# Performance work log

Hardware: AMD Instinct MI355X
Metric: run time of the kernel (lower is better)

The kernel has to match this reference:

```python
import jax, jax.numpy as jnp
import numpy as np

N_NODES = 50000
N_EDGES = 800000
DIM = 128
BN_EPS = 1e-5  # torch.nn.BatchNorm1d default


def _lin_init(k, fan_in, fan_out):
    kw, kb = jax.random.split(k)
    s = 1.0 / np.sqrt(fan_in)
    W = jax.random.uniform(kw, (fan_in, fan_out), jnp.float32, -s, s)
    b = jax.random.uniform(kb, (fan_out,), jnp.float32, -s, s)
    return W, b


def setup_inputs() -> dict:
    key = jax.random.key(0)
    ks = jax.random.split(key, 8)
    d = {}
    d['h'] = jax.random.normal(ks[0], (N_NODES, DIM), jnp.float32)
    d['e'] = jax.random.normal(ks[1], (N_EDGES, DIM), jnp.float32)
    d['src'] = jax.random.randint(ks[2], (N_EDGES,), 0, N_NODES)
    d['dst'] = jax.random.randint(ks[3], (N_EDGES,), 0, N_NODES)
    # mlp_atom: Linear(128,128) -> ReLU -> Linear(128,128)
    d['Wa1'], d['ba1'] = _lin_init(ks[4], DIM, DIM)
    d['Wa2'], d['ba2'] = _lin_init(ks[5], DIM, DIM)
    # mlp_bond
    d['Wb1'], d['bb1'] = _lin_init(ks[6], DIM, DIM)
    d['Wb2'], d['bb2'] = _lin_init(ks[7], DIM, DIM)
    # BatchNorm1d affine params
    d['gamma_a'] = jnp.ones((DIM,), jnp.float32)
    d['beta_a'] = jnp.zeros((DIM,), jnp.float32)
    d['gamma_b'] = jnp.ones((DIM,), jnp.float32)
    d['beta_b'] = jnp.zeros((DIM,), jnp.float32)
    return d


def _mlp(x, W1, b1, W2, b2):
    return jax.nn.relu(x @ W1 + b1) @ W2 + b2


def _bn(x, gamma, beta):
    # training-mode batch norm over the node/edge axis
    mu = jnp.mean(x, axis=0)
    var = jnp.var(x, axis=0)
    return (x - mu) * jax.lax.rsqrt(var + BN_EPS) * gamma + beta


def reference(h, e, src, dst, Wa1, ba1, Wa2, ba2, Wb1, bb1, Wb2, bb2,
              gamma_a, beta_a, gamma_b, beta_b):
    # --- bond (edge) update: GIN-style sum of endpoint atom feats + bond feat
    me = h[src] + h[dst] + e                      # [E, D] irregular gather
    e_new = _bn(_mlp(me, Wb1, bb1, Wb2, bb2), gamma_b, beta_b)
    e_new = e_new + e                             # residual (dropout=Identity)
    # --- atom (node) update: sum-aggregate incident bond feats
    agg = jax.ops.segment_sum(e_new, dst, num_segments=N_NODES)  # [N, D] scatter
    h_new = _bn(_mlp(h + agg, Wa1, ba1, Wa2, ba2), gamma_a, beta_a)
    h_new = h_new + h                             # residual
    return h_new, e_new
```

## Files before the change

kernel.cpp:

```cpp
#include <hip/hip_runtime.h>
#include <cstddef>

#define NN 50000
#define NE 800000
#define D 128
#define BN_EPS 1e-5f

typedef __attribute__((ext_vector_type(8))) short bf16x8;
typedef __attribute__((ext_vector_type(4))) float f32x4;
typedef __attribute__((ext_vector_type(4))) unsigned short us4;

__device__ __forceinline__ unsigned short f2bf(float x) {
    unsigned u = __float_as_uint(x);
    return (unsigned short)((u + 0x7fffu + ((u >> 16) & 1u)) >> 16);
}
__device__ __forceinline__ float bf2f(unsigned short b) {
    return __uint_as_float(((unsigned)b) << 16);
}

__global__ __launch_bounds__(256) void wprep_kernel(
    const float* __restrict__ W, unsigned short* __restrict__ Wt)
{
    const int idx = blockIdx.x * 256 + threadIdx.x;
    const int j  = idx & 7;
    const int l  = (idx >> 3) & 63;
    const int ks = (idx >> 9) & 3;
    const int ct = (idx >> 11) & 7;
    const int n  = 16 * ct + (l & 15);
    const int k  = 32 * ks + ((l >> 4) << 3) + j;
    Wt[idx] = f2bf(W[k * 128 + n]);
}

template<int MODE>
__global__ __launch_bounds__(256, 2) void mlp_mfma_kernel(
    const float* __restrict__ h, const float* __restrict__ e_or_agg,
    const int* __restrict__ src, const int* __restrict__ dst,
    const unsigned short* __restrict__ Wt1, const float* __restrict__ b1,
    const unsigned short* __restrict__ Wt2, const float* __restrict__ b2,
    float* __restrict__ x2out, float* __restrict__ stats)
{
    __shared__ __align__(16) unsigned short Xh[8192];
    __shared__ __align__(16) unsigned short Xl[8192];
    __shared__ __align__(16) float OUTB[64 * 132];

    const int tid  = threadIdx.x;
    const int lane = tid & 63;
    const int w    = tid >> 6;
    const int cg   = tid & 31;
    const int rg   = tid >> 5;
    const int c0   = cg * 4;
    const long r0  = (long)blockIdx.x * 64;

    const bf16x8* Wg1 = (const bf16x8*)Wt1;
    bf16x8 wf[8][4];
#pragma unroll
    for (int ct = 0; ct < 8; ++ct)
#pragma unroll
        for (int ks = 0; ks < 4; ++ks)
            wf[ct][ks] = Wg1[(ct * 4 + ks) * 64 + lane];

#pragma unroll
    for (int p = 0; p < 8; ++p) {
        const int  row  = p * 8 + rg;
        const long grow = r0 + row;
        float4 v = make_float4(0.f, 0.f, 0.f, 0.f);
        if (MODE == 0) {
            const int sN = src[grow];
            const int dN = dst[grow];
            const float4 ev = *(const float4*)(e_or_agg + (size_t)grow * D + c0);
            const float4 hs = *(const float4*)(h + (size_t)sN * D + c0);
            const float4 hd = *(const float4*)(h + (size_t)dN * D + c0);
            v.x = ev.x + hs.x + hd.x; v.y = ev.y + hs.y + hd.y;
            v.z = ev.z + hs.z + hd.z; v.w = ev.w + hs.w + hd.w;
        } else {
            if (grow < NN) {
                const float4 hv = *(const float4*)(h + (size_t)grow * D + c0);
                const float4 av = *(const float4*)(e_or_agg + (size_t)grow * D + c0);
                v.x = hv.x + av.x; v.y = hv.y + av.y;
                v.z = hv.z + av.z; v.w = hv.w + av.w;
            }
        }
        us4 hi, lo;
        hi.x = f2bf(v.x); lo.x = f2bf(v.x - bf2f(hi.x));
        hi.y = f2bf(v.y); lo.y = f2bf(v.y - bf2f(hi.y));
        hi.z = f2bf(v.z); lo.z = f2bf(v.z - bf2f(hi.z));
        hi.w = f2bf(v.w); lo.w = f2bf(v.w - bf2f(hi.w));
        const int addr = row * 128 + (((c0 >> 3) ^ (row & 7)) << 3) + (c0 & 7);
        *(us4*)&Xh[addr] = hi;
        *(us4*)&Xl[addr] = lo;
    }
    __syncthreads();

    const int arow = 16 * w + (lane & 15);
    bf16x8 ah[4], al[4];
#pragma unroll
    for (int ks = 0; ks < 4; ++ks) {
        const int col0  = 32 * ks + ((lane >> 4) << 3);
        const int aaddr = arow * 128 + (((col0 >> 3) ^ (arow & 7)) << 3);
        ah[ks] = *(const bf16x8*)&Xh[aaddr];
        al[ks] = *(const bf16x8*)&Xl[aaddr];
    }
    f32x4 acc[8];
#pragma unroll
    for (int ct = 0; ct < 8; ++ct) acc[ct] = (f32x4){0.f, 0.f, 0.f, 0.f};
#pragma unroll
    for (int ct = 0; ct < 8; ++ct)
#pragma unroll
        for (int ks = 0; ks < 4; ++ks) {
            acc[ct] = __builtin_amdgcn_mfma_f32_16x16x32_bf16(ah[ks], wf[ct][ks], acc[ct], 0, 0, 0);
            acc[ct] = __builtin_amdgcn_mfma_f32_16x16x32_bf16(al[ks], wf[ct][ks], acc[ct], 0, 0, 0);
        }

    const bf16x8* Wg2 = (const bf16x8*)Wt2;
#pragma unroll
    for (int ct = 0; ct < 8; ++ct)
#pragma unroll
        for (int ks = 0; ks < 4; ++ks)
            wf[ct][ks] = Wg2[(ct * 4 + ks) * 64 + lane];

#pragma unroll
    for (int ct = 0; ct < 8; ++ct) {
        const float b1c = b1[16 * ct + (lane & 15)];
#pragma unroll
        for (int r = 0; r < 4; ++r) {
            const int row = 16 * w + ((lane >> 4) << 2) + r;
            OUTB[row * 132 + 16 * ct + (lane & 15)] = fmaxf(acc[ct][r] + b1c, 0.f);
        }
    }
    __syncthreads();

#pragma unroll
    for (int p = 0; p < 8; ++p) {
        const int row = p * 8 + rg;
        const float4 v = *(const float4*)&OUTB[row * 132 + c0];
        us4 hi, lo;
        hi.x = f2bf(v.x); lo.x = f2bf(v.x - bf2f(hi.x));
        hi.y = f2bf(v.y); lo.y = f2bf(v.y - bf2f(hi.y));
        hi.z = f2bf(v.z); lo.z = f2bf(v.z - bf2f(hi.z));
        hi.w = f2bf(v.w); lo.w = f2bf(v.w - bf2f(hi.w));
        const int addr = row * 128 + (((c0 >> 3) ^ (row & 7)) << 3) + (c0 & 7);
        *(us4*)&Xh[addr] = hi;
        *(us4*)&Xl[addr] = lo;
    }
    __syncthreads();

#pragma unroll
    for (int ks = 0; ks < 4; ++ks) {
        const int col0  = 32 * ks + ((lane >> 4) << 3);
        const int aaddr = arow * 128 + (((col0 >> 3) ^ (arow & 7)) << 3);
        ah[ks] = *(const bf16x8*)&Xh[aaddr];
        al[ks] = *(const bf16x8*)&Xl[aaddr];
    }
    f32x4 a2[8];
#pragma unroll
    for (int ct = 0; ct < 8; ++ct) a2[ct] = (f32x4){0.f, 0.f, 0.f, 0.f};
#pragma unroll
    for (int ct = 0; ct < 8; ++ct)
#pragma unroll
        for (int ks = 0; ks < 4; ++ks) {
            a2[ct] = __builtin_amdgcn_mfma_f32_16x16x32_bf16(ah[ks], wf[ct][ks], a2[ct], 0, 0, 0);
            a2[ct] = __builtin_amdgcn_mfma_f32_16x16x32_bf16(al[ks], wf[ct][ks], a2[ct], 0, 0, 0);
        }

#pragma unroll
    for (int ct = 0; ct < 8; ++ct) {
        const float b2c = b2[16 * ct + (lane & 15)];
#pragma unroll
        for (int r = 0; r < 4; ++r) {
            const int row = 16 * w + ((lane >> 4) << 2) + r;
            OUTB[row * 132 + 16 * ct + (lane & 15)] = a2[ct][r] + b2c;
        }
    }
    __syncthreads();

    float ts[4] = {0.f, 0.f, 0.f, 0.f};
    float tq[4] = {0.f, 0.f, 0.f, 0.f};
#pragma unroll
    for (int p = 0; p < 8; ++p) {
        const int  row  = p * 8 + rg;
        const long grow = r0 + row;
        if (MODE == 1 && grow >= NN) continue;
        const float4 v = *(const float4*)&OUTB[row * 132 + c0];
        *(float4*)(x2out + (size_t)grow * D + c0) = v;
        ts[0] += v.x; ts[1] += v.y; ts[2] += v.z; ts[3] += v.w;
        tq[0] += v.x * v.x; tq[1] += v.y * v.y;
        tq[2] += v.z * v.z; tq[3] += v.w * v.w;
    }

    float* red = (float*)Xh;
    *(float4*)&red[rg * 128 + c0]        = make_float4(ts[0], ts[1], ts[2], ts[3]);
    *(float4*)&red[2048 + rg * 128 + c0] = make_float4(tq[0], tq[1], tq[2], tq[3]);
    __syncthreads();
    if (tid < 128) {
        float s = 0.f, q = 0.f;
#pragma unroll
        for (int g = 0; g < 8; ++g) {
            s += red[g * 128 + tid];
            q += red[2048 + g * 128 + tid];
        }
        unsafeAtomicAdd(&stats[tid], s);
        unsafeAtomicAdd(&stats[128 + tid], q);
    }
}

__global__ void bn_finalize_kernel(float* __restrict__ stats,
                                   const float* __restrict__ gamma,
                                   const float* __restrict__ beta,
                                   float inv_count)
{
    const int c = threadIdx.x;
    if (c < D) {
        const float mu  = stats[c] * inv_count;
        const float var = stats[128 + c] * inv_count - mu * mu;
        const float sc  = rsqrtf(var + BN_EPS) * gamma[c];
        stats[256 + c] = sc;
        stats[384 + c] = beta[c] - mu * sc;
    }
}

__global__ __launch_bounds__(256) void hist_kernel(
    const int* __restrict__ dst, int* __restrict__ cnt)
{
    const int i = blockIdx.x * 256 + threadIdx.x;
    if (i < NE) atomicAdd(&cnt[dst[i]], 1);
}

__global__ __launch_bounds__(1024) void scan_kernel(
    const int* __restrict__ cnt, int* __restrict__ off)
{
    __shared__ int part[1024];
    const int t = threadIdx.x;
    const int SEG = (NN + 1023) / 1024;
    const int base = t * SEG;

    int s = 0;
    for (int i = 0; i < SEG; ++i) {
        const int idx = base + i;
        if (idx < NN) s += cnt[idx];
    }
    part[t] = s;
    __syncthreads();
    for (int d = 1; d < 1024; d <<= 1) {
        int v = (t >= d) ? part[t - d] : 0;
        __syncthreads();
        part[t] += v;
        __syncthreads();
    }
    int run = (t > 0) ? part[t - 1] : 0;
    for (int i = 0; i < SEG; ++i) {
        const int idx = base + i;
        if (idx < NN) { off[idx] = run; run += cnt[idx]; }
    }
    if (t == 1023) off[NN] = part[1023];
}

__global__ __launch_bounds__(256) void csr_scatter_kernel(
    const int* __restrict__ dst, const int* __restrict__ off,
    int* __restrict__ cnt, int* __restrict__ csr)
{
    const int i = blockIdx.x * 256 + threadIdx.x;
    if (i < NE) {
        const int d = dst[i];
        const int p = atomicSub(&cnt[d], 1) - 1;
        csr[off[d] + p] = i;
    }
}

__global__ __launch_bounds__(256) void apply_gather_kernel(
    const float* __restrict__ e, const float* __restrict__ stats,
    const int* __restrict__ off, const int* __restrict__ csr,
    float* __restrict__ eout, float* __restrict__ agg)
{
    const int node = blockIdx.x * 4 + (threadIdx.x >> 6);
    const int lane = threadIdx.x & 63;
    const int c0   = lane * 2;
    if (node >= NN) return;

    const float2 sc = *(const float2*)(stats + 256 + c0);
    const float2 sh = *(const float2*)(stats + 384 + c0);
    float2 acc = make_float2(0.f, 0.f);
    const int jb = off[node], je = off[node + 1];
    for (int j = jb; j < je; ++j) {
        const int eidx = csr[j];
        const size_t base = (size_t)eidx * D + c0;
        const float2 x  = *(const float2*)(eout + base);
        const float2 ev = *(const float2*)(e + base);
        float2 v;
        v.x = fmaf(x.x, sc.x, sh.x) + ev.x;
        v.y = fmaf(x.y, sc.y, sh.y) + ev.y;
        *(float2*)(eout + base) = v;
        acc.x += v.x;
        acc.y += v.y;
    }
    *(float2*)(agg + (size_t)node * D + c0) = acc;
}

__global__ __launch_bounds__(256) void node_apply_kernel(
    const float* __restrict__ h, const float* __restrict__ stats,
    float* __restrict__ hout)
{
    const int gid = blockIdx.x * 256 + threadIdx.x;
    const int c0  = (gid & 31) * 4;
    const size_t base = (size_t)(gid >> 5) * D + c0;

    const float4 sc = *(const float4*)(stats + 256 + c0);
    const float4 sh = *(const float4*)(stats + 384 + c0);
    const float4 x  = *(const float4*)(hout + base);
    const float4 hv = *(const float4*)(h + base);
    float4 v;
    v.x = fmaf(x.x, sc.x, sh.x) + hv.x;
    v.y = fmaf(x.y, sc.y, sh.y) + hv.y;
    v.z = fmaf(x.z, sc.z, sh.z) + hv.z;
    v.w = fmaf(x.w, sc.w, sh.w) + hv.w;
    *(float4*)(hout + base) = v;
}

extern "C" void kernel_launch(void* const* d_in, const int* in_sizes, int n_in,
                              void* d_out, int out_size, void* d_ws, size_t ws_size,
                              hipStream_t stream)
{
    const float* h   = (const float*)d_in[0];
    const float* e   = (const float*)d_in[1];
    const int*   src = (const int*)d_in[2];
    const int*   dst = (const int*)d_in[3];
    const float* Wa1 = (const float*)d_in[4];
    const float* ba1 = (const float*)d_in[5];
    const float* Wa2 = (const float*)d_in[6];
    const float* ba2 = (const float*)d_in[7];
    const float* Wb1 = (const float*)d_in[8];
    const float* bb1 = (const float*)d_in[9];
    const float* Wb2 = (const float*)d_in[10];
    const float* bb2 = (const float*)d_in[11];
    const float* ga  = (const float*)d_in[12];
    const float* bea = (const float*)d_in[13];
    const float* gb  = (const float*)d_in[14];
    const float* beb = (const float*)d_in[15];

    float* out  = (float*)d_out;
    float* hnew = out;
    float* enew = out + (size_t)NN * D;

    float* ws     = (float*)d_ws;
    float* estats = ws;
    float* nstats = ws + 512;
    int*   icnt   = (int*)(ws + 1024);
    int*   ioff   = icnt + NN;
    unsigned short* wtb1 = (unsigned short*)(ioff + NN + 1 + 3);
    unsigned short* wtb2 = wtb1 + 16384;
    unsigned short* wta1 = wtb2 + 16384;
    unsigned short* wta2 = wta1 + 16384;
    int*   icsr  = (int*)(wta2 + 16384);
    float* agg   = (float*)(icsr + NE);

    hipMemsetAsync(d_ws, 0, (size_t)(1024 + NN) * sizeof(float), stream);

    wprep_kernel<<<64, 256, 0, stream>>>(Wb1, wtb1);
    wprep_kernel<<<64, 256, 0, stream>>>(Wb2, wtb2);
    wprep_kernel<<<64, 256, 0, stream>>>(Wa1, wta1);
    wprep_kernel<<<64, 256, 0, stream>>>(Wa2, wta2);

    hist_kernel<<<(NE + 255) / 256, 256, 0, stream>>>(dst, icnt);
    scan_kernel<<<1, 1024, 0, stream>>>(icnt, ioff);
    csr_scatter_kernel<<<(NE + 255) / 256, 256, 0, stream>>>(dst, ioff, icnt, icsr);

    mlp_mfma_kernel<0><<<NE / 64, 256, 0, stream>>>(h, e, src, dst,
                                                    wtb1, bb1, wtb2, bb2,
                                                    enew , estats);
    bn_finalize_kernel<<<1, 128, 0, stream>>>(estats, gb, beb, 1.0f / NE);
    apply_gather_kernel<<<(NN + 3) / 4, 256, 0, stream>>>(e, estats, ioff, icsr,
                                                          enew, agg);

    mlp_mfma_kernel<1><<<(NN + 63) / 64, 256, 0, stream>>>(h, agg, nullptr, nullptr,
                                                           wta1, ba1, wta2, ba2,
                                                           hnew , nstats);
    bn_finalize_kernel<<<1, 128, 0, stream>>>(nstats, ga, bea, 1.0f / NN);
    node_apply_kernel<<<(NN * 32) / 256, 256, 0, stream>>>(h, nstats, hnew);
}
```

Baseline: 851.8 us.

## Compute MLP in registers with transposed MFMA and lane shuffles, dropping LDS staging

Restructures the fused MLP kernel so each lane loads its input rows directly into MFMA fragments. The first layer is computed transposed (weights as A, activations as B), so the hidden activations can be repacked into the A operand of the second layer with cross-lane shuffles instead of a round trip through shared memory. W1 is staged in LDS once per block and W2 is read from global per MFMA. The output tile is written straight from the accumulators, BN stats are reduced with shuffles, and the LDS footprint is cut to allow 4 blocks per CU. This removes several syncthreads and LDS passes, at the cost of uncoalesced 4-byte output stores, many shuffles, and repeated global weight loads.

```diff
diff --git a/kernel.cpp b/kernel.cpp
--- a/kernel.cpp
+++ b/kernel.cpp
@@ -8,7 +8,8 @@
 
 typedef __attribute__((ext_vector_type(8))) short bf16x8;
 typedef __attribute__((ext_vector_type(4))) float f32x4;
-typedef __attribute__((ext_vector_type(4))) unsigned short us4;
+
+union FragU { int4 i; bf16x8 v; };
 
 __device__ __forceinline__ unsigned short f2bf(float x) {
     unsigned u = __float_as_uint(x);
@@ -16,6 +17,9 @@
 }
 __device__ __forceinline__ float bf2f(unsigned short b) {
     return __uint_as_float(((unsigned)b) << 16);
+}
+__device__ __forceinline__ unsigned pk2(float a, float b) {
+    return (unsigned)f2bf(a) | ((unsigned)f2bf(b) << 16);
 }
 
 __global__ __launch_bounds__(256) void wprep_kernel(
@@ -32,172 +36,160 @@
 }
 
 template<int MODE>
-__global__ __launch_bounds__(256, 2) void mlp_mfma_kernel(
+__global__ __launch_bounds__(256, 4) void mlp_mfma_kernel(
     const float* __restrict__ h, const float* __restrict__ e_or_agg,
     const int* __restrict__ src, const int* __restrict__ dst,
     const unsigned short* __restrict__ Wt1, const float* __restrict__ b1,
     const unsigned short* __restrict__ Wt2, const float* __restrict__ b2,
     float* __restrict__ x2out, float* __restrict__ stats)
 {
-    __shared__ __align__(16) unsigned short Xh[8192];
-    __shared__ __align__(16) unsigned short Xl[8192];
-    __shared__ __align__(16) float OUTB[64 * 132];
+    __shared__ __align__(16) unsigned short W1L[16384];
+    __shared__ float red[1024];
 
     const int tid  = threadIdx.x;
     const int lane = tid & 63;
     const int w    = tid >> 6;
-    const int cg   = tid & 31;
-    const int rg   = tid >> 5;
-    const int c0   = cg * 4;
+    const int g    = lane >> 4;
+    const int m    = lane & 15;
     const long r0  = (long)blockIdx.x * 64;
 
-    const bf16x8* Wg1 = (const bf16x8*)Wt1;
-    bf16x8 wf[8][4];
+    {
+        int4* dp = (int4*)W1L;
+        const int4* sp = (const int4*)Wt1;
+#pragma unroll
+        for (int i = 0; i < 8; ++i) dp[tid + 256 * i] = sp[tid + 256 * i];
+    }
+    __syncthreads();
+
+    const long rowg = r0 + 16 * w + m;
+    long rowl = rowg;
+    if (MODE == 1) rowl = (rowl < NN) ? rowl : (NN - 1);
+
+    const float *pa, *pb, *pc;
+    if (MODE == 0) {
+        pa = e_or_agg + (size_t)rowg * D;
+        pb = h + (size_t)src[rowg] * D;
+        pc = h + (size_t)dst[rowg] * D;
+    } else {
+        pa = h + (size_t)rowl * D;
+        pb = e_or_agg + (size_t)rowl * D;
+        pc = nullptr;
+    }
+
+    FragU xh[4], xl[4];
+#pragma unroll
+    for (int ks = 0; ks < 4; ++ks) {
+        const int c = 32 * ks + 8 * g;
+        const float4 aa = *(const float4*)(pa + c);
+        const float4 ab = *(const float4*)(pa + c + 4);
+        const float4 ba = *(const float4*)(pb + c);
+        const float4 bb = *(const float4*)(pb + c + 4);
+        float xs[8];
+        xs[0] = aa.x + ba.x; xs[1] = aa.y + ba.y; xs[2] = aa.z + ba.z; xs[3] = aa.w + ba.w;
+        xs[4] = ab.x + bb.x; xs[5] = ab.y + bb.y; xs[6] = ab.z + bb.z; xs[7] = ab.w + bb.w;
+        if (MODE == 0) {
+            const float4 ca = *(const float4*)(pc + c);
+            const float4 cb = *(const float4*)(pc + c + 4);
+            xs[0] += ca.x; xs[1] += ca.y; xs[2] += ca.z; xs[3] += ca.w;
+            xs[4] += cb.x; xs[5] += cb.y; xs[6] += cb.z; xs[7] += cb.w;
+        }
+        const unsigned h0 = pk2(xs[0], xs[1]), h1 = pk2(xs[2], xs[3]);
+        const unsigned h2 = pk2(xs[4], xs[5]), h3 = pk2(xs[6], xs[7]);
+        xh[ks].i = make_int4(h0, h1, h2, h3);
+        float lo[8];
+        lo[0] = xs[0] - bf2f((unsigned short)h0);  lo[1] = xs[1] - bf2f((unsigned short)(h0 >> 16));
+        lo[2] = xs[2] - bf2f((unsigned short)h1);  lo[3] = xs[3] - bf2f((unsigned short)(h1 >> 16));
+        lo[4] = xs[4] - bf2f((unsigned short)h2);  lo[5] = xs[5] - bf2f((unsigned short)(h2 >> 16));
+        lo[6] = xs[6] - bf2f((unsigned short)h3);  lo[7] = xs[7] - bf2f((unsigned short)(h3 >> 16));
+        xl[ks].i = make_int4(pk2(lo[0], lo[1]), pk2(lo[2], lo[3]),
+                             pk2(lo[4], lo[5]), pk2(lo[6], lo[7]));
+    }
+
+    const bf16x8* W1f = (const bf16x8*)W1L;
+    f32x4 acc[8];
+#pragma unroll
+    for (int ct = 0; ct < 8; ++ct) acc[ct] = (f32x4){0.f, 0.f, 0.f, 0.f};
 #pragma unroll
     for (int ct = 0; ct < 8; ++ct)
 #pragma unroll
-        for (int ks = 0; ks < 4; ++ks)
-            wf[ct][ks] = Wg1[(ct * 4 + ks) * 64 + lane];
-
-#pragma unroll
-    for (int p = 0; p < 8; ++p) {
-        const int  row  = p * 8 + rg;
-        const long grow = r0 + row;
-        float4 v = make_float4(0.f, 0.f, 0.f, 0.f);
-        if (MODE == 0) {
-            const int sN = src[grow];
-            const int dN = dst[grow];
-            const float4 ev = *(const float4*)(e_or_agg + (size_t)grow * D + c0);
-            const float4 hs = *(const float4*)(h + (size_t)sN * D + c0);
-            const float4 hd = *(const float4*)(h + (size_t)dN * D + c0);
-            v.x = ev.x + hs.x + hd.x; v.y = ev.y + hs.y + hd.y;
-            v.z = ev.z + hs.z + hd.z; v.w = ev.w + hs.w + hd.w;
-        } else {
-            if (grow < NN) {
-                const float4 hv = *(const float4*)(h + (size_t)grow * D + c0);
-                const float4 av = *(const float4*)(e_or_agg + (size_t)grow * D + c0);
-                v.x = hv.x + av.x; v.y = hv.y + av.y;
-                v.z = hv.z + av.z; v.w = hv.w + av.w;
+        for (int ks = 0; ks < 4; ++ks) {
+            const bf16x8 wf = W1f[(ct * 4 + ks) * 64 + lane];
+            acc[ct] = __builtin_amdgcn_mfma_f32_16x16x32_bf16(wf, xh[ks].v, acc[ct], 0, 0, 0);
+            acc[ct] = __builtin_amdgcn_mfma_f32_16x16x32_bf16(wf, xl[ks].v, acc[ct], 0, 0, 0);
+        }
+
+    unsigned yh[8][2], yl[8][2];
+#pragma unroll
+    for (int ct = 0; ct < 8; ++ct) {
+        const float4 bv = *(const float4*)(b1 + 16 * ct + 4 * g);
+        const float y0 = fmaxf(acc[ct][0] + bv.x, 0.f);
+        const float y1 = fmaxf(acc[ct][1] + bv.y, 0.f);
+        const float y2 = fmaxf(acc[ct][2] + bv.z, 0.f);
+        const float y3 = fmaxf(acc[ct][3] + bv.w, 0.f);
+        yh[ct][0] = pk2(y0, y1);  yh[ct][1] = pk2(y2, y3);
+        const float l0 = y0 - bf2f((unsigned short)yh[ct][0]);
+        const float l1 = y1 - bf2f((unsigned short)(yh[ct][0] >> 16));
+        const float l2 = y2 - bf2f((unsigned short)yh[ct][1]);
+        const float l3 = y3 - bf2f((unsigned short)(yh[ct][1] >> 16));
+        yl[ct][0] = pk2(l0, l1);  yl[ct][1] = pk2(l2, l3);
+    }
+
+    FragU ah[4], al[4];
+    const int sA = ((g & 1) << 5) | m;
+    const int sB = sA + 16;
+    const bool gh = (g >> 1) != 0;
+#pragma unroll
+    for (int ks = 0; ks < 4; ++ks) {
+        int p, q, w0, w1, w2, w3;
+        p = __shfl((int)yh[2*ks][0], sA); q = __shfl((int)yh[2*ks+1][0], sA); w0 = gh ? q : p;
+        p = __shfl((int)yh[2*ks][1], sA); q = __shfl((int)yh[2*ks+1][1], sA); w1 = gh ? q : p;
+        p = __shfl((int)yh[2*ks][0], sB); q = __shfl((int)yh[2*ks+1][0], sB); w2 = gh ? q : p;
+        p = __shfl((int)yh[2*ks][1], sB); q = __shfl((int)yh[2*ks+1][1], sB); w3 = gh ? q : p;
+        ah[ks].i = make_int4(w0, w1, w2, w3);
+        p = __shfl((int)yl[2*ks][0], sA); q = __shfl((int)yl[2*ks+1][0], sA); w0 = gh ? q : p;
+        p = __shfl((int)yl[2*ks][1], sA); q = __shfl((int)yl[2*ks+1][1], sA); w1 = gh ? q : p;
+        p = __shfl((int)yl[2*ks][0], sB); q = __shfl((int)yl[2*ks+1][0], sB); w2 = gh ? q : p;
+        p = __shfl((int)yl[2*ks][1], sB); q = __shfl((int)yl[2*ks+1][1], sB); w3 = gh ? q : p;
+        al[ks].i = make_int4(w0, w1, w2, w3);
+    }
+
+    const bf16x8* W2f = (const bf16x8*)Wt2;
+    f32x4 acc2[8];
+#pragma unroll
+    for (int ct = 0; ct < 8; ++ct) acc2[ct] = (f32x4){0.f, 0.f, 0.f, 0.f};
+#pragma unroll
+    for (int ct = 0; ct < 8; ++ct)
+#pragma unroll
+        for (int ks = 0; ks < 4; ++ks) {
+            const bf16x8 wf = W2f[(ct * 4 + ks) * 64 + lane];
+            acc2[ct] = __builtin_amdgcn_mfma_f32_16x16x32_bf16(ah[ks].v, wf, acc2[ct], 0, 0, 0);
+            acc2[ct] = __builtin_amdgcn_mfma_f32_16x16x32_bf16(al[ks].v, wf, acc2[ct], 0, 0, 0);
+        }
+
+#pragma unroll
+    for (int ct = 0; ct < 8; ++ct) {
+        const float b2c = b2[16 * ct + m];
+        float s = 0.f, q = 0.f;
+#pragma unroll
+        for (int r = 0; r < 4; ++r) {
+            const long grow = r0 + 16 * w + 4 * g + r;
+            if (MODE == 0 || grow < NN) {
+                const float z = acc2[ct][r] + b2c;
+                x2out[(size_t)grow * D + 16 * ct + m] = z;
+                s += z; q += z * z;
             }
         }
-        us4 hi, lo;
-        hi.x = f2bf(v.x); lo.x = f2bf(v.x - bf2f(hi.x));
-        hi.y = f2bf(v.y); lo.y = f2bf(v.y - bf2f(hi.y));
-        hi.z = f2bf(v.z); lo.z = f2bf(v.z - bf2f(hi.z));
-        hi.w = f2bf(v.w); lo.w = f2bf(v.w - bf2f(hi.w));
-        const int addr = row * 128 + (((c0 >> 3) ^ (row & 7)) << 3) + (c0 & 7);
-        *(us4*)&Xh[addr] = hi;
-        *(us4*)&Xl[addr] = lo;
-    }
-    __syncthreads();
-
-    const int arow = 16 * w + (lane & 15);
-    bf16x8 ah[4], al[4];
-#pragma unroll
-    for (int ks = 0; ks < 4; ++ks) {
-        const int col0  = 32 * ks + ((lane >> 4) << 3);
-        const int aaddr = arow * 128 + (((col0 >> 3) ^ (arow & 7)) << 3);
-        ah[ks] = *(const bf16x8*)&Xh[aaddr];
-        al[ks] = *(const bf16x8*)&Xl[aaddr];
-    }
-    f32x4 acc[8];
-#pragma unroll
-    for (int ct = 0; ct < 8; ++ct) acc[ct] = (f32x4){0.f, 0.f, 0.f, 0.f};
-#pragma unroll
-    for (int ct = 0; ct < 8; ++ct)
-#pragma unroll
-        for (int ks = 0; ks < 4; ++ks) {
-            acc[ct] = __builtin_amdgcn_mfma_f32_16x16x32_bf16(ah[ks], wf[ct][ks], acc[ct], 0, 0, 0);
-            acc[ct] = __builtin_amdgcn_mfma_f32_16x16x32_bf16(al[ks], wf[ct][ks], acc[ct], 0, 0, 0);
-        }
-
-    const bf16x8* Wg2 = (const bf16x8*)Wt2;
-#pragma unroll
-    for (int ct = 0; ct < 8; ++ct)
-#pragma unroll
-        for (int ks = 0; ks < 4; ++ks)
-            wf[ct][ks] = Wg2[(ct * 4 + ks) * 64 + lane];
-
-#pragma unroll
-    for (int ct = 0; ct < 8; ++ct) {
-        const float b1c = b1[16 * ct + (lane & 15)];
-#pragma unroll
-        for (int r = 0; r < 4; ++r) {
-            const int row = 16 * w + ((lane >> 4) << 2) + r;
-            OUTB[row * 132 + 16 * ct + (lane & 15)] = fmaxf(acc[ct][r] + b1c, 0.f);
-        }
-    }
-    __syncthreads();
-
-#pragma unroll
-    for (int p = 0; p < 8; ++p) {
-        const int row = p * 8 + rg;
-        const float4 v = *(const float4*)&OUTB[row * 132 + c0];
-        us4 hi, lo;
-        hi.x = f2bf(v.x); lo.x = f2bf(v.x - bf2f(hi.x));
-        hi.y = f2bf(v.y); lo.y = f2bf(v.y - bf2f(hi.y));
-        hi.z = f2bf(v.z); lo.z = f2bf(v.z - bf2f(hi.z));
-        hi.w = f2bf(v.w); lo.w = f2bf(v.w - bf2f(hi.w));
-        const int addr = row * 128 + (((c0 >> 3) ^ (row & 7)) << 3) + (c0 & 7);
-        *(us4*)&Xh[addr] = hi;
-        *(us4*)&Xl[addr] = lo;
-    }
-    __syncthreads();
-
-#pragma unroll
-    for (int ks = 0; ks < 4; ++ks) {
-        const int col0  = 32 * ks + ((lane >> 4) << 3);
-        const int aaddr = arow * 128 + (((col0 >> 3) ^ (arow & 7)) << 3);
-        ah[ks] = *(const bf16x8*)&Xh[aaddr];
-        al[ks] = *(const bf16x8*)&Xl[aaddr];
-    }
-    f32x4 a2[8];
-#pragma unroll
-    for (int ct = 0; ct < 8; ++ct) a2[ct] = (f32x4){0.f, 0.f, 0.f, 0.f};
-#pragma unroll
-    for (int ct = 0; ct < 8; ++ct)
-#pragma unroll
-        for (int ks = 0; ks < 4; ++ks) {
-            a2[ct] = __builtin_amdgcn_mfma_f32_16x16x32_bf16(ah[ks], wf[ct][ks], a2[ct], 0, 0, 0);
-            a2[ct] = __builtin_amdgcn_mfma_f32_16x16x32_bf16(al[ks], wf[ct][ks], a2[ct], 0, 0, 0);
-        }
-
-#pragma unroll
-    for (int ct = 0; ct < 8; ++ct) {
-        const float b2c = b2[16 * ct + (lane & 15)];
-#pragma unroll
-        for (int r = 0; r < 4; ++r) {
-            const int row = 16 * w + ((lane >> 4) << 2) + r;
-            OUTB[row * 132 + 16 * ct + (lane & 15)] = a2[ct][r] + b2c;
-        }
-    }
-    __syncthreads();
-
-    float ts[4] = {0.f, 0.f, 0.f, 0.f};
-    float tq[4] = {0.f, 0.f, 0.f, 0.f};
-#pragma unroll
-    for (int p = 0; p < 8; ++p) {
-        const int  row  = p * 8 + rg;
-        const long grow = r0 + row;
-        if (MODE == 1 && grow >= NN) continue;
-        const float4 v = *(const float4*)&OUTB[row * 132 + c0];
-        *(float4*)(x2out + (size_t)grow * D + c0) = v;
-        ts[0] += v.x; ts[1] += v.y; ts[2] += v.z; ts[3] += v.w;
-        tq[0] += v.x * v.x; tq[1] += v.y * v.y;
-        tq[2] += v.z * v.z; tq[3] += v.w * v.w;
-    }
-
-    float* red = (float*)Xh;
-    *(float4*)&red[rg * 128 + c0]        = make_float4(ts[0], ts[1], ts[2], ts[3]);
-    *(float4*)&red[2048 + rg * 128 + c0] = make_float4(tq[0], tq[1], tq[2], tq[3]);
+        s += __shfl_xor(s, 16); s += __shfl_xor(s, 32);
+        q += __shfl_xor(q, 16); q += __shfl_xor(q, 32);
+        if (g == 0) {
+            red[w * 128 + 16 * ct + m]       = s;
+            red[512 + w * 128 + 16 * ct + m] = q;
+        }
+    }
     __syncthreads();
     if (tid < 128) {
-        float s = 0.f, q = 0.f;
-#pragma unroll
-        for (int g = 0; g < 8; ++g) {
-            s += red[g * 128 + tid];
-            q += red[2048 + g * 128 + tid];
-        }
+        const float s = red[tid] + red[128 + tid] + red[256 + tid] + red[384 + tid];
+        const float q = red[512 + tid] + red[640 + tid] + red[768 + tid] + red[896 + tid];
         unsafeAtomicAdd(&stats[tid], s);
         unsafeAtomicAdd(&stats[128 + tid], q);
     }
```

Measured after the change: 868.4 us. No clear change (+2.0%).
